# Kernel optimization log

Hardware: AMD Instinct MI355X
Metric: run time of the kernel (lower is better)

## Reference

```python
import jax, jax.numpy as jnp
import numpy as np

K = 4        # Legendre orders / channels
T = 1024     # sequence length (== max_len)
B = 2        # batch
D = 256      # feature dim
THETA = 200.0  # LegT window length; dt = 1/theta


def _make_hippo_legt(N):
    # A_{nk} = -sqrt((2n+1)(2k+1)) * sigma_{nk}; B_n = sqrt(2n+1)
    n = np.arange(N, dtype=np.float64)
    P = np.sqrt(2.0 * n + 1.0)
    PP = P[:, None] * P[None, :]
    diff = n[:, None] - n[None, :]
    sign = np.ones_like(PP)
    upper = diff < 0
    sign[upper] = (-1.0) ** (-diff[upper])
    A = -PP * sign
    Bv = P.reshape(N, 1)
    return A, Bv


def _legt_kernel(T_, N, theta):
    """M[k] = Abar^k @ Bbar, k = 0..T-1 (bilinear discretization, dt=1/theta)."""
    A, Bv = _make_hippo_legt(N)
    dt = 1.0 / float(theta)
    I = np.eye(N)
    inv = np.linalg.inv(I - 0.5 * dt * A)
    Abar = inv @ (I + 0.5 * dt * A)
    Bbar = (inv @ (Bv * dt)).squeeze(-1)
    M = np.zeros((T_, N), dtype=np.float64)
    cur = Bbar.copy()
    for k in range(T_):
        M[k] = cur
        cur = Abar @ cur
    return M.astype(np.float32)


def setup_inputs() -> dict:
    key = jax.random.key(0)
    h = jax.random.normal(key, (B, T, D), dtype=jnp.float32)
    M = jnp.asarray(_legt_kernel(T, K, THETA))  # (T, K) precomputed buffer
    return {"h": h, "M": M}


def reference(h, M):
    # c[b, t, k, d] = sum_{s<=t} M[t-s, k] * h[b, s, d]
    B_, T_, d = h.shape
    t = jnp.arange(T_)
    ix = t[:, None] - t[None, :]                    # (T, T)
    mask = (ix >= 0).astype(h.dtype)
    W = M[jnp.clip(ix, 0)] * mask[:, :, None]       # (T, T, K) causal Toeplitz bank
    return jnp.einsum('tsk,bsd->btkd', W, h)        # (B, T, K, D)
```

## Files before the change

### kernel.cpp

```cpp
#include <hip/hip_runtime.h>
#include <math.h>

namespace {

constexpr int K_ = 4;
constexpr int T_ = 1024;
constexpr int B_ = 2;
constexpr int D_ = 256;
constexpr int NSEQ = B_ * D_;

constexpr int CH = 128;
constexpr int L_ = T_ / CH;
constexpr int LOG_CH = 7;

__device__ __forceinline__ void base_consts(float Af[4][4], float Bf[4]) {
    const double dt = 1.0 / 200.0;
    double P[4], A[4][4];
#pragma unroll
    for (int n = 0; n < 4; ++n) P[n] = sqrt(2.0 * n + 1.0);
#pragma unroll
    for (int n = 0; n < 4; ++n)
#pragma unroll
        for (int k = 0; k < 4; ++k) {
            double s = (n >= k) ? 1.0 : (((k - n) & 1) ? -1.0 : 1.0);
            A[n][k] = -P[n] * P[k] * s;
        }
    double aug[4][9];
#pragma unroll
    for (int r = 0; r < 4; ++r) {
#pragma unroll
        for (int c = 0; c < 4; ++c) {
            double idc = (r == c) ? 1.0 : 0.0;
            aug[r][c]     = idc - 0.5 * dt * A[r][c];
            aug[r][4 + c] = idc + 0.5 * dt * A[r][c];
        }
        aug[r][8] = P[r] * dt;
    }
#pragma unroll
    for (int p = 0; p < 4; ++p) {
        double pinv = 1.0 / aug[p][p];
#pragma unroll
        for (int c = 0; c < 9; ++c) aug[p][c] *= pinv;
#pragma unroll
        for (int r = 0; r < 4; ++r) {
            if (r == p) continue;
            double f = aug[r][p];
#pragma unroll
            for (int c = 0; c < 9; ++c) aug[r][c] -= f * aug[p][c];
        }
    }
#pragma unroll
    for (int r = 0; r < 4; ++r) {
#pragma unroll
        for (int c = 0; c < 4; ++c) Af[r][c] = (float)aug[r][4 + c];
        Bf[r] = (float)aug[r][8];
    }
}

__device__ __forceinline__ void matsq(const float X[4][4], float Y[4][4]) {
#pragma unroll
    for (int r = 0; r < 4; ++r)
#pragma unroll
        for (int c = 0; c < 4; ++c) {
            float acc = 0.f;
#pragma unroll
            for (int k = 0; k < 4; ++k) acc = fmaf(X[r][k], X[k][c], acc);
            Y[r][c] = acc;
        }
}

__device__ __forceinline__ void scan_consts(float AP[LOG_CH][4][4]) {
    float Af[4][4], Bf[4];
    base_consts(Af, Bf);
    float X[4][4], Y[4][4];
    matsq(Af, X);
    matsq(X, Y);
    matsq(Y, X);
#pragma unroll
    for (int s = 0; s < LOG_CH; ++s) {
#pragma unroll
        for (int r = 0; r < 4; ++r)
#pragma unroll
            for (int c = 0; c < 4; ++c) AP[s][r][c] = X[r][c];
        matsq(X, Y);
#pragma unroll
        for (int r = 0; r < 4; ++r)
#pragma unroll
            for (int c = 0; c < 4; ++c) X[r][c] = Y[r][c];
    }
}

__global__ __launch_bounds__(256) void k_scan(
    const float* __restrict__ h, const float* __restrict__ M,
    float* __restrict__ ws_init)
{
    const int sp = threadIdx.x & 1;
    const int c  = threadIdx.x >> 1;
    const int seq = blockIdx.x * 2 + sp;
    const int b = seq >> 8, d = seq & (D_ - 1);

    float AP[LOG_CH][4][4];
    scan_consts(AP);

    const float* hp = h + ((size_t)(b * T_ + c * L_)) * D_ + d;
    float y0 = 0.f, y1 = 0.f, y2 = 0.f, y3 = 0.f;
#pragma unroll
    for (int i = 0; i < L_; ++i) {
        float hv = hp[i * D_];
        const float* mr = M + (L_ - 1 - i) * K_;
        y0 = fmaf(mr[0], hv, y0);
        y1 = fmaf(mr[1], hv, y1);
        y2 = fmaf(mr[2], hv, y2);
        y3 = fmaf(mr[3], hv, y3);
    }
    float4 v = make_float4(y0, y1, y2, y3);

    __shared__ float4 lds[CH * 2];
#pragma unroll
    for (int s = 0; s < LOG_CH; ++s) {
        const int off = 1 << s;
        lds[threadIdx.x] = v;
        __syncthreads();
        if (c >= off) {
            float4 p = lds[threadIdx.x - off * 2];
            v.x = fmaf(AP[s][0][0], p.x, fmaf(AP[s][0][1], p.y, fmaf(AP[s][0][2], p.z, fmaf(AP[s][0][3], p.w, v.x))));
            v.y = fmaf(AP[s][1][0], p.x, fmaf(AP[s][1][1], p.y, fmaf(AP[s][1][2], p.z, fmaf(AP[s][1][3], p.w, v.y))));
            v.z = fmaf(AP[s][2][0], p.x, fmaf(AP[s][2][1], p.y, fmaf(AP[s][2][2], p.z, fmaf(AP[s][2][3], p.w, v.z))));
            v.w = fmaf(AP[s][3][0], p.x, fmaf(AP[s][3][1], p.y, fmaf(AP[s][3][2], p.z, fmaf(AP[s][3][3], p.w, v.w))));
        }
        __syncthreads();
    }
    float4* ip = (float4*)ws_init;
    if (c < CH - 1) ip[(size_t)(c + 1) * NSEQ + seq] = v;
    if (c == 0)     ip[seq] = make_float4(0.f, 0.f, 0.f, 0.f);
}

__global__ __launch_bounds__(256) void k_emit(
    const float* __restrict__ h, const float* __restrict__ ws_init,
    float* __restrict__ out)
{
    const int d = threadIdx.x;
    const int c = blockIdx.x & (CH - 1);
    const int b = blockIdx.x >> LOG_CH;

    float Af[4][4], Bf[4];
    base_consts(Af, Bf);

    float4 xi = ((const float4*)ws_init)[(size_t)c * NSEQ + b * D_ + d];
    float x0 = xi.x, x1 = xi.y, x2 = xi.z, x3 = xi.w;

    const float* hp = h + ((size_t)(b * T_ + c * L_)) * D_ + d;
    float* op = out + ((size_t)(b * T_ + c * L_)) * K_ * D_ + d;
#pragma unroll
    for (int i = 0; i < L_; ++i) {
        float hv = hp[i * D_];
        float n0 = fmaf(Af[0][0], x0, fmaf(Af[0][1], x1, fmaf(Af[0][2], x2, fmaf(Af[0][3], x3, Bf[0] * hv))));
        float n1 = fmaf(Af[1][0], x0, fmaf(Af[1][1], x1, fmaf(Af[1][2], x2, fmaf(Af[1][3], x3, Bf[1] * hv))));
        float n2 = fmaf(Af[2][0], x0, fmaf(Af[2][1], x1, fmaf(Af[2][2], x2, fmaf(Af[2][3], x3, Bf[2] * hv))));
        float n3 = fmaf(Af[3][0], x0, fmaf(Af[3][1], x1, fmaf(Af[3][2], x2, fmaf(Af[3][3], x3, Bf[3] * hv))));
        x0 = n0; x1 = n1; x2 = n2; x3 = n3;
        __builtin_nontemporal_store(x0, &op[0 * D_]);
        __builtin_nontemporal_store(x1, &op[1 * D_]);
        __builtin_nontemporal_store(x2, &op[2 * D_]);
        __builtin_nontemporal_store(x3, &op[3 * D_]);
        op += K_ * D_;
    }
}

}

extern "C" void kernel_launch(void* const* d_in, const int* in_sizes, int n_in,
                              void* d_out, int out_size, void* d_ws, size_t ws_size,
                              hipStream_t stream) {
    const float* h = (const float*)d_in[0];
    const float* M = (const float*)d_in[1];
    float* out = (float*)d_out;

    float* ws_init = (float*)d_ws;

    k_scan<<<NSEQ / 2, 256, 0, stream>>>(h, M, ws_init);
    k_emit<<<B_ * CH, 256, 0, stream>>>(h, ws_init, out);
}
```

Baseline: 63.86 us.

## Restructure chunk scan to pair chunks per thread and coalesce 16 sequences per block

```diff
diff --git a/kernel.cpp b/kernel.cpp
--- a/kernel.cpp
+++ b/kernel.cpp
@@ -12,6 +12,8 @@
 constexpr int CH = 128;
 constexpr int L_ = T_ / CH;
 constexpr int LOG_CH = 7;
+constexpr int NPAIR = CH / 2;
+constexpr int SD = 16;
 
 __device__ __forceinline__ void base_consts(float Af[4][4], float Bf[4]) {
     const double dt = 1.0 / 200.0;
@@ -90,49 +92,85 @@
     }
 }
 
-__global__ __launch_bounds__(256) void k_scan(
+#define MAT_AFF(Mx, i0, i1, i2, i3, o0, o1, o2, o3, s0, s1, s2, s3)            \
+    {                                                                          \
+        o0 = fmaf(Mx[0][0], i0, fmaf(Mx[0][1], i1, fmaf(Mx[0][2], i2, fmaf(Mx[0][3], i3, s0)))); \
+        o1 = fmaf(Mx[1][0], i0, fmaf(Mx[1][1], i1, fmaf(Mx[1][2], i2, fmaf(Mx[1][3], i3, s1)))); \
+        o2 = fmaf(Mx[2][0], i0, fmaf(Mx[2][1], i1, fmaf(Mx[2][2], i2, fmaf(Mx[2][3], i3, s2)))); \
+        o3 = fmaf(Mx[3][0], i0, fmaf(Mx[3][1], i1, fmaf(Mx[3][2], i2, fmaf(Mx[3][3], i3, s3)))); \
+    }
+
+__global__ __launch_bounds__(1024) void k_scan(
     const float* __restrict__ h, const float* __restrict__ M,
     float* __restrict__ ws_init)
 {
-    const int sp = threadIdx.x & 1;
-    const int c  = threadIdx.x >> 1;
-    const int seq = blockIdx.x * 2 + sp;
-    const int b = seq >> 8, d = seq & (D_ - 1);
+    const int tid  = threadIdx.x;
+    const int s16  = tid & (SD - 1);
+    const int c2   = tid >> 4;
+    const int b    = blockIdx.x >> 4;
+    const int d    = (blockIdx.x & 15) * SD + s16;
+    const int seq  = b * D_ + d;
 
     float AP[LOG_CH][4][4];
     scan_consts(AP);
 
-    const float* hp = h + ((size_t)(b * T_ + c * L_)) * D_ + d;
-    float y0 = 0.f, y1 = 0.f, y2 = 0.f, y3 = 0.f;
-#pragma unroll
-    for (int i = 0; i < L_; ++i) {
-        float hv = hp[i * D_];
-        const float* mr = M + (L_ - 1 - i) * K_;
-        y0 = fmaf(mr[0], hv, y0);
-        y1 = fmaf(mr[1], hv, y1);
-        y2 = fmaf(mr[2], hv, y2);
-        y3 = fmaf(mr[3], hv, y3);
-    }
-    float4 v = make_float4(y0, y1, y2, y3);
-
-    __shared__ float4 lds[CH * 2];
-#pragma unroll
-    for (int s = 0; s < LOG_CH; ++s) {
+    float mc[L_][K_];
+#pragma unroll
+    for (int i = 0; i < L_; ++i) {
+        const float4 mr = ((const float4*)M)[L_ - 1 - i];
+        mc[i][0] = mr.x; mc[i][1] = mr.y; mc[i][2] = mr.z; mc[i][3] = mr.w;
+    }
+
+    const float* hp = h + ((size_t)(b * T_ + c2 * 2 * L_)) * D_ + d;
+    float e0 = 0.f, e1 = 0.f, e2 = 0.f, e3 = 0.f;
+    float o0 = 0.f, o1 = 0.f, o2 = 0.f, o3 = 0.f;
+#pragma unroll
+    for (int i = 0; i < L_; ++i) {
+        const float hv = hp[i * D_];
+        e0 = fmaf(mc[i][0], hv, e0);
+        e1 = fmaf(mc[i][1], hv, e1);
+        e2 = fmaf(mc[i][2], hv, e2);
+        e3 = fmaf(mc[i][3], hv, e3);
+    }
+#pragma unroll
+    for (int i = 0; i < L_; ++i) {
+        const float hv = hp[(L_ + i) * D_];
+        o0 = fmaf(mc[i][0], hv, o0);
+        o1 = fmaf(mc[i][1], hv, o1);
+        o2 = fmaf(mc[i][2], hv, o2);
+        o3 = fmaf(mc[i][3], hv, o3);
+    }
+    float4 v;
+    MAT_AFF(AP[0], e0, e1, e2, e3, v.x, v.y, v.z, v.w, o0, o1, o2, o3);
+
+    __shared__ float4 lds[NPAIR * SD];
+#pragma unroll
+    for (int s = 0; s < 6; ++s) {
         const int off = 1 << s;
-        lds[threadIdx.x] = v;
+        lds[tid] = v;
         __syncthreads();
-        if (c >= off) {
-            float4 p = lds[threadIdx.x - off * 2];
-            v.x = fmaf(AP[s][0][0], p.x, fmaf(AP[s][0][1], p.y, fmaf(AP[s][0][2], p.z, fmaf(AP[s][0][3], p.w, v.x))));
-            v.y = fmaf(AP[s][1][0], p.x, fmaf(AP[s][1][1], p.y, fmaf(AP[s][1][2], p.z, fmaf(AP[s][1][3], p.w, v.y))));
-            v.z = fmaf(AP[s][2][0], p.x, fmaf(AP[s][2][1], p.y, fmaf(AP[s][2][2], p.z, fmaf(AP[s][2][3], p.w, v.z))));
-            v.w = fmaf(AP[s][3][0], p.x, fmaf(AP[s][3][1], p.y, fmaf(AP[s][3][2], p.z, fmaf(AP[s][3][3], p.w, v.w))));
+        if (c2 >= off) {
+            const float4 p = lds[tid - off * SD];
+            const float4 t = v;
+            MAT_AFF(AP[s + 1], p.x, p.y, p.z, p.w, v.x, v.y, v.z, v.w,
+                    t.x, t.y, t.z, t.w);
         }
         __syncthreads();
     }
+
+    lds[tid] = v;
+    __syncthreads();
+    float q0 = 0.f, q1 = 0.f, q2 = 0.f, q3 = 0.f;
+    if (c2 > 0) {
+        const float4 p = lds[tid - SD];
+        q0 = p.x; q1 = p.y; q2 = p.z; q3 = p.w;
+    }
+    float r0, r1, r2, r3;
+    MAT_AFF(AP[0], q0, q1, q2, q3, r0, r1, r2, r3, e0, e1, e2, e3);
+
     float4* ip = (float4*)ws_init;
-    if (c < CH - 1) ip[(size_t)(c + 1) * NSEQ + seq] = v;
-    if (c == 0)     ip[seq] = make_float4(0.f, 0.f, 0.f, 0.f);
+    ip[(size_t)(2 * c2)     * NSEQ + seq] = make_float4(q0, q1, q2, q3);
+    ip[(size_t)(2 * c2 + 1) * NSEQ + seq] = make_float4(r0, r1, r2, r3);
 }
 
 __global__ __launch_bounds__(256) void k_emit(
@@ -178,6 +216,6 @@
 
     float* ws_init = (float*)d_ws;
 
-    k_scan<<<NSEQ / 2, 256, 0, stream>>>(h, M, ws_init);
+    k_scan<<<NSEQ / SD, NPAIR * SD, 0, stream>>>(h, M, ws_init);
     k_emit<<<B_ * CH, 256, 0, stream>>>(h, ws_init, out);
 }
```

Result: no change. 63.16 us (-1.1%).
